# Kernel tuning notes

Measured on AMD Instinct MI355X. Metric: run time of the kernel, lower is better.

The kernel has to match this reference:

```python
import jax, jax.numpy as jnp
import numpy as np
import math

B, S, H, NH, R = 1, 1024, 4096, 32, 16
HD = H // NH
BLOCK = 64
PRUNE_RATIO = 0.5
NF4_TABLE = jnp.array([
    -1.0, -0.6961928009986877, -0.5250730514526367, -0.39491748809814453,
    -0.28444138169288635, -0.18477343022823334, -0.09105003625154495, 0.0,
    0.07958029955625534, 0.16093020141124725, 0.24611230194568634,
    0.33791524171829224, 0.4407098591327667, 0.5626170039176941,
    0.7229568362236023, 1.0], dtype=jnp.float32)


def dequant_nf4(codes, absmax):
    # codes: [out,in] int4 values in [0,16); absmax: per-64-elem block scale
    vals = NF4_TABLE[codes.reshape(-1)]                 # [out*in]
    vals = vals.reshape(-1, BLOCK) * absmax[:, None]    # blockwise rescale
    return vals.reshape(codes.shape)                    # [out,in]


def setup_inputs() -> dict:
    key = jax.random.key(0)
    ks = jax.random.split(key, 32)
    d = {"x": jax.random.normal(ks[0], (B, S, H), dtype=jnp.float32)}
    i = 1
    for n in ("q", "k", "v", "o"):
        d[f"w_{n}_codes"] = jax.random.randint(ks[i], (H, H), 0, 16, dtype=jnp.int32); i += 1
        d[f"w_{n}_absmax"] = jax.random.uniform(ks[i], (H * H // BLOCK,), dtype=jnp.float32) * 0.06; i += 1
        d[f"b_{n}"] = jax.random.normal(ks[i], (H,), dtype=jnp.float32) * 0.01; i += 1
        d[f"w_{n}_lora_a"] = jax.random.normal(ks[i], (H, R), dtype=jnp.float32) * (1.0 / math.sqrt(H)); i += 1
        d[f"w_{n}_lora_b"] = jax.random.normal(ks[i], (R, H), dtype=jnp.float32) * 0.02; i += 1
    causal = jnp.tril(jnp.ones((S, S), dtype=bool))
    d["attention_mask"] = jnp.where(causal, 0.0, -1e9).astype(jnp.float32)[None, None]
    return d


def _proj(x, codes, absmax, b, la, lb):
    w = dequant_nf4(codes, absmax).T          # [in,out]
    main = x @ w + b
    lora_a = x @ la                            # [B,S,R]
    return main + lora_a @ lb, main, lora_a


def _kth_val(t, use_abs=True):
    flat = jnp.abs(t).ravel() if use_abs else t.ravel()
    k = int(t.size * PRUNE_RATIO)
    return jnp.sort(flat)[k - 1]


def reference(x, w_q_codes, w_q_absmax, b_q, w_q_lora_a, w_q_lora_b,
              w_k_codes, w_k_absmax, b_k, w_k_lora_a, w_k_lora_b,
              w_v_codes, w_v_absmax, b_v, w_v_lora_a, w_v_lora_b,
              w_o_codes, w_o_absmax, b_o, w_o_lora_a, w_o_lora_b,
              attention_mask):
    q, _, _ = _proj(x, w_q_codes, w_q_absmax, b_q, w_q_lora_a, w_q_lora_b)
    k, _, _ = _proj(x, w_k_codes, w_k_absmax, b_k, w_k_lora_a, w_k_lora_b)
    v, _, _ = _proj(x, w_v_codes, w_v_absmax, b_v, w_v_lora_a, w_v_lora_b)
    # [B,S,H] -> [B,NH,S,HD]
    qh = q.reshape(B, S, NH, HD).transpose(0, 2, 1, 3)
    kh = k.reshape(B, S, NH, HD).transpose(0, 2, 1, 3)
    vh = v.reshape(B, S, NH, HD).transpose(0, 2, 1, 3)
    s = jnp.einsum("bhqd,bhkd->bhqk", qh, kh) / math.sqrt(HD) + attention_mask
    a = jax.nn.softmax(s, axis=-1)
    o = jnp.einsum("bhqk,bhkd->bhqd", a, vh)
    o = o.transpose(0, 2, 1, 3).reshape(B, S, H)
    o_final, _, _ = _proj(o, w_o_codes, w_o_absmax, b_o, w_o_lora_a, w_o_lora_b)
    # iteration < 10 branch: magnitude-pruning thresholds via kth smallest value
    kth_vals = jnp.stack([
        _kth_val(x), _kth_val(qh), _kth_val(kh), _kth_val(vh),
        _kth_val(a, use_abs=False), _kth_val(o)])
    return o_final, kth_vals
```

## Files before the change

kernel.cpp:

```cpp
#include <hip/hip_runtime.h>

#define S_LEN  1024
#define H_DIM  4096
#define NHEAD  32
#define HEAD_D 128
#define RANK   16
#define KE3    4160
#define KEO    4160
#define TOTP   ((long)NHEAD * S_LEN * S_LEN)

typedef __bf16 bf16x8 __attribute__((ext_vector_type(8)));
typedef float  f32x4  __attribute__((ext_vector_type(4)));
typedef unsigned short ushort8v __attribute__((ext_vector_type(8)));

#define GLOAD_LDS16(g, l) __builtin_amdgcn_global_load_lds( \
    (const __attribute__((address_space(1))) unsigned int*)(g), \
    (__attribute__((address_space(3))) unsigned int*)(l), 16, 0, 0)

__device__ const float NF4_TAB[16] = {
    -1.0f, -0.6961928009986877f, -0.5250730514526367f, -0.39491748809814453f,
    -0.28444138169288635f, -0.18477343022823334f, -0.09105003625154495f, 0.0f,
    0.07958029955625534f, 0.16093020141124725f, 0.24611230194568634f,
    0.33791524171829224f, 0.4407098591327667f, 0.5626170039176941f,
    0.7229568362236023f, 1.0f};

__device__ __forceinline__ unsigned short f2bf(float f) {
    unsigned int u = __builtin_bit_cast(unsigned int, f);
    u = (u + 0x7FFFu + ((u >> 16) & 1u)) >> 16;
    return (unsigned short)u;
}

__device__ __forceinline__ float bf2f(unsigned short s) {
    return __builtin_bit_cast(float, (unsigned int)s << 16);
}

__device__ __forceinline__ void dequant_body(
    const int* __restrict__ codes, const float* __restrict__ absmax,
    unsigned short* __restrict__ out, long i, int ostride) {
    int4 c0 = *(const int4*)(codes + i);
    int4 c1 = *(const int4*)(codes + i + 4);
    float am = absmax[i >> 6];
    long orow = i >> 12;
    int  col  = (int)(i & 4095);
    ushort8v r;
    r[0] = f2bf(NF4_TAB[c0.x] * am);
    r[1] = f2bf(NF4_TAB[c0.y] * am);
    r[2] = f2bf(NF4_TAB[c0.z] * am);
    r[3] = f2bf(NF4_TAB[c0.w] * am);
    r[4] = f2bf(NF4_TAB[c1.x] * am);
    r[5] = f2bf(NF4_TAB[c1.y] * am);
    r[6] = f2bf(NF4_TAB[c1.z] * am);
    r[7] = f2bf(NF4_TAB[c1.w] * am);
    *(ushort8v*)(out + orow * ostride + col) = r;
}

__global__ __launch_bounds__(256) void xcast_lora(
    const float* __restrict__ x, const float* __restrict__ la0,
    const float* __restrict__ la1, const float* __restrict__ la2,
    unsigned short* __restrict__ xb_ext) {
    __shared__ float xs[4096];
    int m = (int)blockIdx.x;
    int tid = threadIdx.x;
    const float* xr = x + (long)m * H_DIM;
    int c = tid * 16;
    float4 f0 = *(const float4*)(xr + c);
    float4 f1 = *(const float4*)(xr + c + 4);
    float4 f2 = *(const float4*)(xr + c + 8);
    float4 f3 = *(const float4*)(xr + c + 12);
    *(float4*)(xs + c)      = f0;
    *(float4*)(xs + c + 4)  = f1;
    *(float4*)(xs + c + 8)  = f2;
    *(float4*)(xs + c + 12) = f3;
    ushort8v r0, r1;
    r0[0] = f2bf(f0.x); r0[1] = f2bf(f0.y); r0[2] = f2bf(f0.z); r0[3] = f2bf(f0.w);
    r0[4] = f2bf(f1.x); r0[5] = f2bf(f1.y); r0[6] = f2bf(f1.z); r0[7] = f2bf(f1.w);
    r1[0] = f2bf(f2.x); r1[1] = f2bf(f2.y); r1[2] = f2bf(f2.z); r1[3] = f2bf(f2.w);
    r1[4] = f2bf(f3.x); r1[5] = f2bf(f3.y); r1[6] = f2bf(f3.z); r1[7] = f2bf(f3.w);
    unsigned short* orow = xb_ext + (long)m * KE3 + c;
    *(ushort8v*)orow = r0;
    *(ushort8v*)(orow + 8) = r1;
    __syncthreads();
    int w = tid >> 6, lane = tid & 63;
    if (w < 3) {
        const float* la = (w == 0) ? la0 : (w == 1) ? la1 : la2;
        float s[16];
#pragma unroll
        for (int r = 0; r < 16; ++r) s[r] = 0.f;
        for (int k = lane; k < H_DIM; k += 64) {
            float xv = xs[k];
            const float4* lr = (const float4*)(la + (long)k * RANK);
            float4 q0 = lr[0], q1 = lr[1], q2 = lr[2], q3 = lr[3];
            s[0] += xv * q0.x;  s[1] += xv * q0.y;  s[2] += xv * q0.z;  s[3] += xv * q0.w;
            s[4] += xv * q1.x;  s[5] += xv * q1.y;  s[6] += xv * q1.z;  s[7] += xv * q1.w;
            s[8] += xv * q2.x;  s[9] += xv * q2.y;  s[10] += xv * q2.z; s[11] += xv * q2.w;
            s[12] += xv * q3.x; s[13] += xv * q3.y; s[14] += xv * q3.z; s[15] += xv * q3.w;
        }
        for (int off = 32; off; off >>= 1)
#pragma unroll
            for (int r = 0; r < 16; ++r) s[r] += __shfl_xor(s[r], off);
        if (lane == 0)
#pragma unroll
            for (int r = 0; r < 16; ++r)
                xb_ext[(long)m * KE3 + 4096 + 16 * w + r] = f2bf(s[r]);
    } else if (lane < 16) {
        xb_ext[(long)m * KE3 + 4144 + lane] = 0;
    }
}

__global__ __launch_bounds__(256) void prep_weights(
    const int* __restrict__ c0, const int* __restrict__ c1,
    const int* __restrict__ c2, const int* __restrict__ c3,
    const float* __restrict__ a0, const float* __restrict__ a1,
    const float* __restrict__ a2, const float* __restrict__ a3,
    const float* __restrict__ lb0, const float* __restrict__ lb1,
    const float* __restrict__ lb2, const float* __restrict__ lb3,
    const float* __restrict__ b0, const float* __restrict__ b1,
    const float* __restrict__ b2,
    unsigned short* __restrict__ wqkv, unsigned short* __restrict__ wo,
    float* __restrict__ bias3, unsigned int* __restrict__ hist, long n) {
    int p = blockIdx.y;
    long bx = blockIdx.x;
    int tid = threadIdx.x;
    if (bx < 8192) {
        const int* codes = (p == 0) ? c0 : (p == 1) ? c1 : (p == 2) ? c2 : c3;
        const float* am  = (p == 0) ? a0 : (p == 1) ? a1 : (p == 2) ? a2 : a3;
        long i = (bx * 256 + tid) * 8;
        if (i >= n) return;
        if (p < 3) dequant_body(codes, am, wqkv + (size_t)p * H_DIM * KE3, i, KE3);
        else       dequant_body(codes, am, wo, i, KEO);
        return;
    }
    if (bx < 9216) {
        long g = (bx - 8192) * 256 + tid;
        int row = (int)(g >> 6), c = (int)(g & 63);
        if (p < 3) {
            const float* lb = (p == 0) ? lb0 : (p == 1) ? lb1 : lb2;
            unsigned int r = (unsigned int)(c - 16 * p);
            float v = (r < 16u) ? lb[r * H_DIM + row] : 0.f;
            wqkv[(size_t)p * H_DIM * KE3 + (long)row * KE3 + 4096 + c] = f2bf(v);
            if (g < H_DIM) {
                const float* bp = (p == 0) ? b0 : (p == 1) ? b1 : b2;
                bias3[(size_t)p * H_DIM + g] = bp[g];
            }
            return;
        }
        float v = (c < 16) ? lb3[c * H_DIM + row] : 0.f;
        wo[(long)row * KEO + 4096 + c] = f2bf(v);
        return;
    }
    if (p == 1) {
        long g = (bx - 9216) * 256 + tid;
        if (g < 6 * 16384) hist[g] = 0u;
    }
}

__global__ __launch_bounds__(256) void lora_ao_kernel(
    unsigned short* __restrict__ ob_ext, const float* __restrict__ la) {
    int m = blockIdx.x;
    const unsigned short* xr = ob_ext + (long)m * KEO;
    int tid = threadIdx.x, lane = tid & 63, wid = tid >> 6;
    float s[4] = {0.f, 0.f, 0.f, 0.f};
    for (int k = lane; k < H_DIM; k += 64) {
        float xv = bf2f(xr[k]);
        const float* lr = la + (long)k * RANK + wid * 4;
        s[0] += xv * lr[0]; s[1] += xv * lr[1];
        s[2] += xv * lr[2]; s[3] += xv * lr[3];
    }
    for (int off = 32; off; off >>= 1)
        for (int r = 0; r < 4; ++r) s[r] += __shfl_down(s[r], off);
    if (lane == 0) {
        for (int r = 0; r < 4; ++r)
            ob_ext[(long)m * KEO + 4096 + wid * 4 + r] = f2bf(s[r]);
        for (int r = 0; r < 12; ++r)
            ob_ext[(long)m * KEO + 4112 + wid * 12 + r] = 0;
    }
}

template<int MODE>
__global__ __launch_bounds__(256) void gemm_nt(
    const unsigned short* __restrict__ A, const unsigned short* __restrict__ B,
    void* __restrict__ Cv, void* __restrict__ Cv2, const float* __restrict__ bias,
    int K, int lda, int ldb, int ldc,
    long strideA, long strideB, long strideC, float alpha,
    const unsigned short* __restrict__ tsrc, unsigned short* __restrict__ tdst) {
    __shared__ unsigned short As[128][64];
    __shared__ unsigned short Bs[128][64];
    const int tid = threadIdx.x;
    int bm, bn;
    int k0s = 0, k0e = K;
    if (MODE == 1) {
        int i = blockIdx.x;
        if (i >= 36) {
            unsigned short (*tl)[33] = (unsigned short(*)[33])&As[0][0];
            int tb = (i - 36) + 4 * blockIdx.z;
            int tx = tid & 31, ty = tid >> 5;
            for (int tile = tb; tile < 4096; tile += 128) {
                int tc = tile & 127, ts = tile >> 7;
                int c0 = tc * 32, s0 = ts * 32;
                for (int j = 0; j < 32; j += 8)
                    tl[ty + j][tx] = tsrc[(long)(s0 + ty + j) * H_DIM + c0 + tx];
                __syncthreads();
                for (int j = 0; j < 32; j += 8)
                    tdst[(long)(c0 + ty + j) * S_LEN + s0 + tx] = tl[tx][ty + j];
                __syncthreads();
            }
            return;
        }
        int tm = (int)((sqrtf(8.f * i + 1.f) - 1.f) * 0.5f);
        if ((tm + 1) * (tm + 2) / 2 <= i) tm++;
        if (tm * (tm + 1) / 2 > i) tm--;
        int tn = i - tm * (tm + 1) / 2;
        bm = tm * 128; bn = tn * 128;
    } else {
        bm = blockIdx.y * 128; bn = blockIdx.x * 128;
        if (MODE == 2) { int kl = bm + 128; if (kl < k0e) k0e = kl; }
    }
    const unsigned short* Ab = A;
    const unsigned short* Bb = B;
    long coff = 0;
    void* Cuse = Cv;
    if (MODE == 3) {
        int Kh = (K / 2) & ~63;
        k0s = blockIdx.z ? Kh : 0;
        k0e = blockIdx.z ? K : Kh;
        Cuse = blockIdx.z ? Cv2 : Cv;
    } else {
        Ab += (long)blockIdx.z * strideA;
        Bb += (long)blockIdx.z * strideB;
        coff = (long)blockIdx.z * strideC;
    }
    const int lane = tid & 63, wid = tid >> 6;
    const int wm = (wid >> 1) * 64, wn = (wid & 1) * 64;
    const int srow = lane >> 3;
    const int scol = ((lane & 7) ^ srow) << 3;
    const int r0 = wid * 8 + srow;
    const unsigned short* gA0 = Ab + (long)(bm + r0) * lda + scol;
    const unsigned short* gB0 = Bb + (long)(bn + r0) * ldb + scol;
    f32x4 acc[4][4] = {};
    const int q = lane >> 4, rr = lane & 15;
    const int colh0 = ((q ^ (rr & 7)) << 3);
    const int colh1 = colh0 ^ 32;
    for (int k0 = k0s; k0 < k0e; k0 += 64) {
#pragma unroll
        for (int p = 0; p < 4; ++p) {
            GLOAD_LDS16(gA0 + (long)p * 32 * lda + k0, &As[p * 32 + wid * 8][0]);
            GLOAD_LDS16(gB0 + (long)p * 32 * ldb + k0, &Bs[p * 32 + wid * 8][0]);
        }
        __syncthreads();
        bf16x8 af[4], bfr[4];
#pragma unroll
        for (int i = 0; i < 4; ++i) {
            af[i]  = __builtin_bit_cast(bf16x8, *(const uint4*)&As[wm + i * 16 + rr][colh0]);
            bfr[i] = __builtin_bit_cast(bf16x8, *(const uint4*)&Bs[wn + i * 16 + rr][colh0]);
        }
#pragma unroll
        for (int i = 0; i < 4; ++i)
#pragma unroll
            for (int j = 0; j < 4; ++j)
                acc[i][j] = __builtin_amdgcn_mfma_f32_16x16x32_bf16(
                    af[i], bfr[j], acc[i][j], 0, 0, 0);
#pragma unroll
        for (int i = 0; i < 4; ++i) {
            af[i]  = __builtin_bit_cast(bf16x8, *(const uint4*)&As[wm + i * 16 + rr][colh1]);
            bfr[i] = __builtin_bit_cast(bf16x8, *(const uint4*)&Bs[wn + i * 16 + rr][colh1]);
        }
#pragma unroll
        for (int i = 0; i < 4; ++i)
#pragma unroll
            for (int j = 0; j < 4; ++j)
                acc[i][j] = __builtin_amdgcn_mfma_f32_16x16x32_bf16(
                    af[i], bfr[j], acc[i][j], 0, 0, 0);
        __syncthreads();
    }
    const int cr = (lane >> 4) * 4;
    const int cc = lane & 15;
    float bv[4];
#pragma unroll
    for (int j = 0; j < 4; ++j)
        bv[j] = bias ? bias[(long)blockIdx.z * H_DIM + bn + wn + j * 16 + cc] : 0.f;
    if (MODE != 3) {
        unsigned short* Cb = (unsigned short*)Cuse + coff;
        for (int i = 0; i < 4; ++i)
            for (int j = 0; j < 4; ++j) {
                unsigned short* cp = Cb + (long)(bm + wm + i * 16 + cr) * ldc
                                        + (bn + wn + j * 16 + cc);
                for (int r = 0; r < 4; ++r)
                    cp[(long)r * ldc] = f2bf(acc[i][j][r] * alpha + bv[j]);
            }
    } else {
        float* Cb = (float*)Cuse + coff;
        for (int i = 0; i < 4; ++i)
            for (int j = 0; j < 4; ++j) {
                float* cp = Cb + (long)(bm + wm + i * 16 + cr) * ldc
                               + (bn + wn + j * 16 + cc);
                for (int r = 0; r < 4; ++r)
                    cp[(long)r * ldc] = acc[i][j][r] * alpha + bv[j];
            }
    }
}

__global__ __launch_bounds__(256) void softmax_causal(unsigned short* __restrict__ scores16) {
    int b = blockIdx.x;
    int h = b >> 9, pr = b & 511;
    int tid = threadIdx.x, lane = tid & 63, wid = tid >> 6;
    __shared__ float red[4], red2[4];
    for (int half = 0; half < 2; ++half) {
        int i = half ? (S_LEN - 1 - pr) : pr;
        unsigned short* row = scores16 + ((long)h * S_LEN + i) * S_LEN;
        int L = i + 1;
        float v[4];
        float mx = -1e30f;
        for (int t = 0; t < 4; ++t) {
            int j = tid + (t << 8);
            v[t] = (j < L) ? bf2f(row[j]) : -1e30f;
            mx = fmaxf(mx, v[t]);
        }
        for (int off = 32; off; off >>= 1) mx = fmaxf(mx, __shfl_xor(mx, off));
        if (lane == 0) red[wid] = mx;
        __syncthreads();
        mx = fmaxf(fmaxf(red[0], red[1]), fmaxf(red[2], red[3]));
        float e[4], sum = 0.f;
        for (int t = 0; t < 4; ++t) {
            int j = tid + (t << 8);
            e[t] = (j < L) ? __expf(v[t] - mx) : 0.f;
            sum += e[t];
        }
        for (int off = 32; off; off >>= 1) sum += __shfl_xor(sum, off);
        if (lane == 0) red2[wid] = sum;
        __syncthreads();
        sum = red2[0] + red2[1] + red2[2] + red2[3];
        float inv = 1.f / sum;
        for (int t = 0; t < 4; ++t) {
            int j = tid + (t << 8);
            row[j] = f2bf(e[t] * inv);
        }
        __syncthreads();
    }
}

__global__ __launch_bounds__(256, 2) void hist6(
    const float* __restrict__ x, const unsigned short* __restrict__ qkv,
    const unsigned short* __restrict__ ob, const unsigned short* __restrict__ P,
    unsigned int* __restrict__ hist) {
    __shared__ unsigned int lh[16384];
    const long SH = (long)S_LEN * H_DIM;
    int t = threadIdx.x;
    int b = blockIdx.x;
    int ten, b0, nblk;
    if (b < 256)      { ten = 0; b0 = 0;   nblk = 256; }
    else if (b < 384) { ten = 1; b0 = 256; nblk = 128; }
    else if (b < 512) { ten = 2; b0 = 384; nblk = 128; }
    else if (b < 640) { ten = 3; b0 = 512; nblk = 128; }
    else if (b < 768) { ten = 4; b0 = 640; nblk = 128; }
    else              { ten = 5; b0 = 768; nblk = 768; }
    unsigned int* gh = hist + (long)ten * 16384;
    for (int k = t; k < 16384; k += 256) lh[k] = 0u;
    __syncthreads();
    long i = (long)(b - b0) * 256 + t;
    long stride = (long)nblk * 256;
    if (ten == 0) {
        for (; i < SH / 4; i += stride) {
            float4 v = *(const float4*)(x + i * 4);
            unsigned int u0 = (__builtin_bit_cast(unsigned int, v.x) & 0x7FFFFFFFu) >> 16;
            unsigned int u1 = (__builtin_bit_cast(unsigned int, v.y) & 0x7FFFFFFFu) >> 16;
            unsigned int u2 = (__builtin_bit_cast(unsigned int, v.z) & 0x7FFFFFFFu) >> 16;
            unsigned int u3 = (__builtin_bit_cast(unsigned int, v.w) & 0x7FFFFFFFu) >> 16;
            atomicAdd(&lh[u0 < 16384u ? u0 : 16383u], 1u);
            atomicAdd(&lh[u1 < 16384u ? u1 : 16383u], 1u);
            atomicAdd(&lh[u2 < 16384u ? u2 : 16383u], 1u);
            atomicAdd(&lh[u3 < 16384u ? u3 : 16383u], 1u);
        }
    } else if (ten <= 3) {
        const unsigned short* src = qkv + (size_t)(ten - 1) * SH;
        for (; i < SH / 8; i += stride) {
            ushort8v v = ((const ushort8v*)src)[i];
#pragma unroll
            for (int j = 0; j < 8; ++j) {
                unsigned int u = v[j] & 0x7FFFu;
                atomicAdd(&lh[u < 16384u ? u : 16383u], 1u);
            }
        }
    } else if (ten == 4) {
        for (; i < SH / 8; i += stride) {
            long off = (i >> 9) * KEO + ((i & 511) << 3);
            ushort8v v = *(const ushort8v*)(ob + off);
#pragma unroll
            for (int j = 0; j < 8; ++j) {
                unsigned int u = v[j] & 0x7FFFu;
                atomicAdd(&lh[u < 16384u ? u : 16383u], 1u);
            }
        }
    } else {
        unsigned int zc = 0;
        for (; i < TOTP / 8; i += stride) {
            ushort8v v = ((const ushort8v*)P)[i];
#pragma unroll
            for (int j = 0; j < 8; ++j) {
                unsigned int bb = v[j];
                if (bb == 0) zc++;
                else atomicAdd(&lh[bb < 16384u ? bb : 16383u], 1u);
            }
        }
        if (zc) atomicAdd(&lh[0], zc);
    }
    __syncthreads();
    for (int k = t; k < 16384; k += 256) {
        unsigned int c = lh[k];
        if (c) atomicAdd(&gh[k], c);
    }
}

__global__ __launch_bounds__(256) void finish_kernel(
    float* __restrict__ out, const float* __restrict__ part,
    const float* __restrict__ bias, const unsigned int* __restrict__ hist,
    float* __restrict__ out_kth) {
    int b = blockIdx.x;
    int t = threadIdx.x;
    if (b < 4096) {
        long idx = ((long)b * 256 + t) * 4;
        int n = (int)(idx & 4095);
        float4 o = *(float4*)(out + idx);
        float4 p = *(const float4*)(part + idx);
        float4 bb = *(const float4*)(bias + n);
        o.x += p.x + bb.x; o.y += p.y + bb.y; o.z += p.z + bb.z; o.w += p.w + bb.w;
        *(float4*)(out + idx) = o;
        return;
    }
    int ten = b - 4096;
    const unsigned int* h = hist + (long)ten * 16384;
    __shared__ unsigned int partl[256];
    unsigned int s = 0;
    for (int bb = 0; bb < 64; ++bb) s += h[t * 64 + bb];
    partl[t] = s;
    __syncthreads();
    if (t == 0) {
        long k = (ten == 5) ? TOTP / 2 : (long)S_LEN * H_DIM / 2;
        long c = 0;
        int ch = 0;
        for (; ch < 256; ++ch) {
            if (c + (long)partl[ch] >= k) break;
            c += partl[ch];
        }
        int bin = ch * 64;
        for (;; ++bin) {
            unsigned int hv = h[bin];
            if (c + (long)hv >= k) break;
            c += hv;
        }
        int slot = (ten == 4) ? 5 : (ten == 5) ? 4 : ten;
        out_kth[slot] = __builtin_bit_cast(float, (unsigned int)bin << 16);
    }
}

extern "C" void kernel_launch(void* const* d_in, const int* in_sizes, int n_in,
                              void* d_out, int out_size, void* d_ws, size_t ws_size,
                              hipStream_t stream) {
    (void)in_sizes; (void)n_in; (void)out_size; (void)ws_size;
    const float* x = (const float*)d_in[0];
    const int*   wcodes[4] = {(const int*)d_in[1], (const int*)d_in[6],
                              (const int*)d_in[11], (const int*)d_in[16]};
    const float* wabs[4]   = {(const float*)d_in[2], (const float*)d_in[7],
                              (const float*)d_in[12], (const float*)d_in[17]};
    const float* bias[4]   = {(const float*)d_in[3], (const float*)d_in[8],
                              (const float*)d_in[13], (const float*)d_in[18]};
    const float* lA[4]     = {(const float*)d_in[4], (const float*)d_in[9],
                              (const float*)d_in[14], (const float*)d_in[19]};
    const float* lB[4]     = {(const float*)d_in[5], (const float*)d_in[10],
                              (const float*)d_in[15], (const float*)d_in[20]};

    char* wp = (char*)d_ws;
    auto alloc = [&](size_t bytes) {
        char* p = wp; wp += (bytes + 255) & ~(size_t)255; return p;
    };
    const size_t SH  = (size_t)S_LEN * H_DIM;
    const long   nW  = (long)H_DIM * H_DIM;
    unsigned short* xb_ext = (unsigned short*)alloc((size_t)S_LEN * KE3 * 2);
    unsigned short* qkvb   = (unsigned short*)alloc(3 * SH * 2);
    unsigned short* vT     = (unsigned short*)alloc(SH * 2);
    unsigned short* ob_ext = (unsigned short*)alloc((size_t)S_LEN * KEO * 2);
    unsigned short* Wd_ext = (unsigned short*)alloc((size_t)H_DIM * KEO * 2);
    float*        opart  = (float*)alloc(SH * 4);
    float*        bias3  = (float*)alloc(3 * H_DIM * 4);
    unsigned int* hist   = (unsigned int*)alloc(6 * 16384 * 4);
    char* bigbuf = alloc((size_t)3 * H_DIM * KE3 * 2);
    unsigned short* Wqkv_ext = (unsigned short*)bigbuf;
    unsigned short* scores16 = (unsigned short*)bigbuf;

    float* out_final = (float*)d_out;
    float* out_kth   = out_final + SH;

    unsigned short* qb = qkvb;
    unsigned short* kb = qkvb + SH;
    unsigned short* vb = qkvb + 2 * SH;

    xcast_lora<<<S_LEN, 256, 0, stream>>>(x, lA[0], lA[1], lA[2], xb_ext);

    prep_weights<<<dim3(9600, 4), 256, 0, stream>>>(
        wcodes[0], wcodes[1], wcodes[2], wcodes[3],
        wabs[0], wabs[1], wabs[2], wabs[3],
        lB[0], lB[1], lB[2], lB[3],
        bias[0], bias[1], bias[2],
        Wqkv_ext, Wd_ext, bias3, hist, nW);

    gemm_nt<0><<<dim3(32, 8, 3), 256, 0, stream>>>(
        xb_ext, Wqkv_ext, qkvb, nullptr, bias3, KE3, KE3, KE3, H_DIM,
        0, (long)H_DIM * KE3, (long)SH, 1.0f, nullptr, nullptr);

    gemm_nt<1><<<dim3(40, 1, NHEAD), 256, 0, stream>>>(
        qb, kb, scores16, nullptr, nullptr, HEAD_D, H_DIM, H_DIM, S_LEN,
        128, 128, (long)S_LEN * S_LEN, 0.08838834764831845f, vb, vT);

    softmax_causal<<<NHEAD * S_LEN / 2, 256, 0, stream>>>(scores16);

    gemm_nt<2><<<dim3(1, 8, NHEAD), 256, 0, stream>>>(
        scores16, vT, ob_ext, nullptr, nullptr, S_LEN,
        S_LEN, S_LEN, KEO,
        (long)S_LEN * S_LEN, (long)HEAD_D * S_LEN, 128, 1.0f, nullptr, nullptr);

    lora_ao_kernel<<<S_LEN, 256, 0, stream>>>(ob_ext, lA[3]);

    gemm_nt<3><<<dim3(32, 8, 2), 256, 0, stream>>>(
        ob_ext, Wd_ext, out_final, opart, nullptr, KEO, KEO, KEO, H_DIM,
        0, 0, 0, 1.0f, nullptr, nullptr);

    hist6<<<1536, 256, 0, stream>>>(x, qkvb, ob_ext, scores16, hist);

    finish_kernel<<<4102, 256, 0, stream>>>(out_final, opart, bias[3], hist, out_kth);
}
```

Before: 722.1 us.

## Double-buffer LDS tiles in gemm_nt to overlap global loads with MFMA

Splits the shared-memory A/B tiles into two buffers and prefetches the next K-tile with global_load_lds while the current tile feeds the MFMAs. Explicit vmcnt waits and raw s_barrier calls, fenced by sched_barrier, replace the __syncthreads pair. The goal is to hide global-memory latency in the projection and attention GEMMs. LDS use per block doubles to 64KB, which can lower occupancy. The hand-written waitcnt and barrier ordering must be exactly right for correctness.

```diff
diff --git a/kernel.cpp b/kernel.cpp
--- a/kernel.cpp
+++ b/kernel.cpp
@@ -183,15 +183,15 @@
     int K, int lda, int ldb, int ldc,
     long strideA, long strideB, long strideC, float alpha,
     const unsigned short* __restrict__ tsrc, unsigned short* __restrict__ tdst) {
-    __shared__ unsigned short As[128][64];
-    __shared__ unsigned short Bs[128][64];
+    __shared__ unsigned short As[2][128][64];
+    __shared__ unsigned short Bs[2][128][64];
     const int tid = threadIdx.x;
     int bm, bn;
     int k0s = 0, k0e = K;
     if (MODE == 1) {
         int i = blockIdx.x;
         if (i >= 36) {
-            unsigned short (*tl)[33] = (unsigned short(*)[33])&As[0][0];
+            unsigned short (*tl)[33] = (unsigned short(*)[33])&As[0][0][0];
             int tb = (i - 36) + 4 * blockIdx.z;
             int tx = tid & 31, ty = tid >> 5;
             for (int tile = tb; tile < 4096; tile += 128) {
@@ -240,18 +240,32 @@
     const int q = lane >> 4, rr = lane & 15;
     const int colh0 = ((q ^ (rr & 7)) << 3);
     const int colh1 = colh0 ^ 32;
-    for (int k0 = k0s; k0 < k0e; k0 += 64) {
+
+    auto STAGE = [&](int buf, int k0) {
 #pragma unroll
         for (int p = 0; p < 4; ++p) {
-            GLOAD_LDS16(gA0 + (long)p * 32 * lda + k0, &As[p * 32 + wid * 8][0]);
-            GLOAD_LDS16(gB0 + (long)p * 32 * ldb + k0, &Bs[p * 32 + wid * 8][0]);
-        }
-        __syncthreads();
+            GLOAD_LDS16(gA0 + (long)p * 32 * lda + k0, &As[buf][p * 32 + wid * 8][0]);
+            GLOAD_LDS16(gB0 + (long)p * 32 * ldb + k0, &Bs[buf][p * 32 + wid * 8][0]);
+        }
+    };
+
+    const int nt = (k0e - k0s) >> 6;
+    STAGE(0, k0s);
+    for (int t = 0; t < nt; ++t) {
+        const int cur = t & 1;
+        if (t + 1 < nt) {
+            STAGE(cur ^ 1, k0s + (t + 1) * 64);
+            asm volatile("s_waitcnt vmcnt(8)" ::: "memory");
+        } else {
+            asm volatile("s_waitcnt vmcnt(0)" ::: "memory");
+        }
+        __builtin_amdgcn_s_barrier();
+        __builtin_amdgcn_sched_barrier(0);
         bf16x8 af[4], bfr[4];
 #pragma unroll
         for (int i = 0; i < 4; ++i) {
-            af[i]  = __builtin_bit_cast(bf16x8, *(const uint4*)&As[wm + i * 16 + rr][colh0]);
-            bfr[i] = __builtin_bit_cast(bf16x8, *(const uint4*)&Bs[wn + i * 16 + rr][colh0]);
+            af[i]  = __builtin_bit_cast(bf16x8, *(const uint4*)&As[cur][wm + i * 16 + rr][colh0]);
+            bfr[i] = __builtin_bit_cast(bf16x8, *(const uint4*)&Bs[cur][wn + i * 16 + rr][colh0]);
         }
 #pragma unroll
         for (int i = 0; i < 4; ++i)
@@ -261,8 +275,8 @@
                     af[i], bfr[j], acc[i][j], 0, 0, 0);
 #pragma unroll
         for (int i = 0; i < 4; ++i) {
-            af[i]  = __builtin_bit_cast(bf16x8, *(const uint4*)&As[wm + i * 16 + rr][colh1]);
-            bfr[i] = __builtin_bit_cast(bf16x8, *(const uint4*)&Bs[wn + i * 16 + rr][colh1]);
+            af[i]  = __builtin_bit_cast(bf16x8, *(const uint4*)&As[cur][wm + i * 16 + rr][colh1]);
+            bfr[i] = __builtin_bit_cast(bf16x8, *(const uint4*)&Bs[cur][wn + i * 16 + rr][colh1]);
         }
 #pragma unroll
         for (int i = 0; i < 4; ++i)
@@ -270,7 +284,8 @@
             for (int j = 0; j < 4; ++j)
                 acc[i][j] = __builtin_amdgcn_mfma_f32_16x16x32_bf16(
                     af[i], bfr[j], acc[i][j], 0, 0, 0);
-        __syncthreads();
+        __builtin_amdgcn_sched_barrier(0);
+        __builtin_amdgcn_s_barrier();
     }
     const int cr = (lane >> 4) * 4;
     const int cc = lane & 15;
```

After: 769.6 us. +6.6%, slower.
